# Kernel optimization log

Hardware: AMD Instinct MI355X
Metric: run time of the kernel (lower is better)

The kernel has to match this reference:

```python
import jax, jax.numpy as jnp
import numpy as np
import math

P, DD, N, E, NDRUGS = 256, 128, 1024, 250000, 200000
BASELINE = 6.0

def _prelu(x, a):
    return jnp.where(x >= 0, x, a * x)

def _lrelu(x):
    return jnp.where(x >= 0, x, 0.2 * x)

def _lin(x, W, b):
    return x @ W.T + b

def setup_inputs() -> dict:
    key = jax.random.key(0)
    ks = jax.random.split(key, 40)
    f32 = jnp.float32
    inp = {}
    inp["target_features"] = jax.random.normal(ks[0], (P,), f32)
    inp["form_features"] = jax.random.normal(ks[1], (N, P), f32)
    inp["role_features"] = jax.random.normal(ks[2], (N, P), f32)
    inp["form_neighbors"] = jnp.arange(N, dtype=jnp.int32)
    inp["form_binds_src"] = jax.random.randint(ks[3], (E,), 0, N, jnp.int32)
    inp["form_binds_dst"] = jax.random.randint(ks[4], (E,), 0, NDRUGS, jnp.int32)
    inp["form_binds_y"] = jax.random.uniform(ks[5], (E,), f32, 4.0, 9.0)
    inp["role_neighbors"] = jnp.arange(N, dtype=jnp.int32)
    inp["role_binds_src"] = jax.random.randint(ks[6], (E,), 0, N, jnp.int32)
    inp["role_binds_dst"] = jax.random.randint(ks[7], (E,), 0, NDRUGS, jnp.int32)
    inp["role_binds_y"] = jax.random.uniform(ks[8], (E,), f32, 4.0, 9.0)
    inp["drug_features"] = jax.random.normal(ks[9], (NDRUGS, DD), f32)
    s = 0.02
    # prot_refiner: Linear(P,P) -> PReLU -> Linear(P,P)
    inp["Wr1"] = jax.random.normal(ks[10], (P, P), f32) * s
    inp["br1"] = jnp.zeros((P,), f32)
    inp["ar1"] = jnp.asarray(0.25, f32)
    inp["Wr2"] = jax.random.normal(ks[11], (P, P), f32) * s
    inp["br2"] = jnp.zeros((P,), f32)
    # q/k/v projections
    inp["Wq"] = jax.random.normal(ks[12], (DD, P), f32) * s
    inp["bq"] = jnp.zeros((DD,), f32)
    inp["Wk"] = jax.random.normal(ks[13], (DD, DD), f32) * s
    inp["bk"] = jnp.zeros((DD,), f32)
    inp["Wv"] = jax.random.normal(ks[14], (DD, DD), f32) * s
    inp["bv"] = jnp.zeros((DD,), f32)
    inp["layer_emb"] = jax.random.normal(ks[15], (2, 16), f32) * s
    # attn_net: (2P+16)->128->64->1 with LeakyReLU(0.2)
    inp["Wa1"] = jax.random.normal(ks[16], (128, 2 * P + 16), f32) * s
    inp["ba1"] = jnp.zeros((128,), f32)
    inp["Wa2"] = jax.random.normal(ks[17], (64, 128), f32) * s
    inp["ba2"] = jnp.zeros((64,), f32)
    inp["Wa3"] = jax.random.normal(ks[18], (1, 64), f32) * s
    inp["ba3"] = jnp.zeros((1,), f32)
    # integration_mlp: Linear(DD,P) -> PReLU -> Linear(P,P)
    inp["Wi1"] = jax.random.normal(ks[19], (P, DD), f32) * s
    inp["bi1"] = jnp.zeros((P,), f32)
    inp["ai"] = jnp.asarray(0.25, f32)
    inp["Wi2"] = jax.random.normal(ks[20], (P, P), f32) * s
    inp["bi2"] = jnp.zeros((P,), f32)
    inp["ln_g"] = jnp.ones((P,), f32)
    inp["ln_b"] = jnp.zeros((P,), f32)
    return inp

def reference(target_features, form_features, role_features, form_neighbors,
              form_binds_src, form_binds_dst, form_binds_y,
              role_neighbors, role_binds_src, role_binds_dst, role_binds_y,
              drug_features,
              Wr1, br1, ar1, Wr2, br2, Wq, bq, Wk, bk, Wv, bv, layer_emb,
              Wa1, ba1, Wa2, ba2, Wa3, ba3, Wi1, bi1, ai, Wi2, bi2, ln_g, ln_b):
    def refine(x):
        return _lin(_prelu(_lin(x, Wr1, br1), ar1), Wr2, br2)

    zt = refine(target_features)          # [P]
    zf = refine(form_features)            # [N, P]
    zr = refine(role_features)            # [N, P]
    Qv = _lin(zt, Wq, bq)                 # [DD]

    def build_msgs(neighbors, src, dst, y):
        # segment id for each edge: position of src in (sorted) neighbor_ids;
        # edges whose src is not a neighbor go to the dummy segment n.
        n = neighbors.shape[0]
        pos = jnp.clip(jnp.searchsorted(neighbors, src), 0, n - 1)
        seg = jnp.where(neighbors[pos] == src, pos, n)
        d = drug_features[dst]                                # [E, DD] gather
        K = _lin(d, Wk, bk)                                   # [E, DD]
        V = _lin(d, Wv, bv) * (y - BASELINE)[:, None]         # [E, DD]
        s = (K @ Qv) / math.sqrt(DD)                          # [E]
        nseg = n + 1
        m = jax.ops.segment_max(s, seg, num_segments=nseg)    # per-neighbor max
        ex = jnp.exp(s - m[seg])                              # stable softmax numerator
        den = jax.ops.segment_sum(ex, seg, num_segments=nseg)[:n]          # [N]
        num = jax.ops.segment_sum(ex[:, None] * V, seg, num_segments=nseg)[:n]  # [N, DD]
        return jnp.where(den[:, None] > 0, num / jnp.maximum(den, 1e-30)[:, None], 0.0)

    form_msgs = build_msgs(form_neighbors, form_binds_src, form_binds_dst, form_binds_y)
    role_msgs = build_msgs(role_neighbors, role_binds_src, role_binds_dst, role_binds_y)

    def attn(zn, layer_id):
        n = zn.shape[0]
        le = jnp.broadcast_to(layer_emb[layer_id], (n, 16))
        zt_e = jnp.broadcast_to(zt, (n, P))
        x = jnp.concatenate([zt_e, zn, le], axis=-1)          # [N, 2P+16]
        h = _lrelu(_lin(x, Wa1, ba1))
        h = _lrelu(_lin(h, Wa2, ba2))
        return _lin(h, Wa3, ba3)                              # [N, 1]

    all_msgs = jnp.concatenate([form_msgs, role_msgs], axis=0)   # [2N, DD]
    all_attn = jnp.concatenate([attn(zf, 0), attn(zr, 1)], axis=0)  # [2N, 1]
    w = jax.nn.softmax(all_attn, axis=0)
    v_prior = jnp.sum(w * all_msgs, axis=0)                   # [DD]
    integ = _lin(_prelu(_lin(v_prior, Wi1, bi1), ai), Wi2, bi2)
    x = zt + integ
    mu = jnp.mean(x, axis=-1, keepdims=True)
    var = jnp.var(x, axis=-1, keepdims=True)
    z = (x - mu) / jnp.sqrt(var + 1e-5) * ln_g + ln_b
    return (z, form_msgs, role_msgs)
```

## Files before the change

### kernel.cpp

```cpp
#include <hip/hip_runtime.h>

#define NP 256
#define NDD 128
#define NN 1024
#define NE 250000
#define SB 62

__global__ __launch_bounds__(256) void refine_qk_kernel(
    const float* __restrict__ tgt, const float* __restrict__ formf, const float* __restrict__ rolef,
    const float* __restrict__ Wr1, const float* __restrict__ br1, const float* __restrict__ ar1,
    const float* __restrict__ Wr2, const float* __restrict__ br2,
    const float* __restrict__ Wq, const float* __restrict__ bq,
    const float* __restrict__ Wk, const float* __restrict__ bk,
    float* __restrict__ zt, float* __restrict__ zf, float* __restrict__ zr,
    float* __restrict__ qk, float* __restrict__ s0,
    int* __restrict__ count, int* __restrict__ cursor0)
{
  __shared__ float X[4][NP];
  __shared__ float H[4][NP];
  __shared__ float Zs[NP];
  __shared__ float Q[NDD];
  __shared__ float red[NDD];
  const int t = threadIdx.x;
  const int base = blockIdx.x * 4;

  if (blockIdx.x == 1){
    #pragma unroll
    for (int i = 0; i < 8; i++) count[t + i*256] = 0;
  } else if (blockIdx.x == 2){
    #pragma unroll
    for (int i = 0; i < 8; i++) cursor0[t + i*256] = 0;
  }

  #pragma unroll
  for (int r = 0; r < 4; r++){
    int row = base + r;
    if (row < 2*NN + 1){
      const float* xp;
      if (row == 0)        xp = tgt;
      else if (row <= NN)  xp = formf + (size_t)(row-1)*NP;
      else                 xp = rolef + (size_t)(row-NN-1)*NP;
      X[r][t] = xp[t];
    } else {
      X[r][t] = 0.f;
    }
  }
  __syncthreads();
  const float a1 = ar1[0];
  float acc[4];
  #pragma unroll
  for (int r = 0; r < 4; r++) acc[r] = 0.f;
  const float4* w1p = reinterpret_cast<const float4*>(Wr1) + t*(NP/4);
  for (int k4 = 0; k4 < NP/4; k4++){
    float4 w = w1p[k4];
    #pragma unroll
    for (int r = 0; r < 4; r++){
      float4 xv = *reinterpret_cast<const float4*>(&X[r][k4*4]);
      acc[r] = fmaf(w.x, xv.x, acc[r]);
      acc[r] = fmaf(w.y, xv.y, acc[r]);
      acc[r] = fmaf(w.z, xv.z, acc[r]);
      acc[r] = fmaf(w.w, xv.w, acc[r]);
    }
  }
  const float b1 = br1[t];
  #pragma unroll
  for (int r = 0; r < 4; r++){
    float h = acc[r] + b1;
    H[r][t] = h >= 0.f ? h : a1*h;
  }
  __syncthreads();
  #pragma unroll
  for (int r = 0; r < 4; r++) acc[r] = 0.f;
  const float4* w2p = reinterpret_cast<const float4*>(Wr2) + t*(NP/4);
  for (int k4 = 0; k4 < NP/4; k4++){
    float4 w = w2p[k4];
    #pragma unroll
    for (int r = 0; r < 4; r++){
      float4 hv = *reinterpret_cast<const float4*>(&H[r][k4*4]);
      acc[r] = fmaf(w.x, hv.x, acc[r]);
      acc[r] = fmaf(w.y, hv.y, acc[r]);
      acc[r] = fmaf(w.z, hv.z, acc[r]);
      acc[r] = fmaf(w.w, hv.w, acc[r]);
    }
  }
  const float b2 = br2[t];
  #pragma unroll
  for (int r = 0; r < 4; r++){
    int row = base + r;
    if (row < 2*NN + 1){
      float v = acc[r] + b2;
      float* op;
      if (row == 0){ op = zt; Zs[t] = v; }
      else if (row <= NN)  op = zf + (size_t)(row-1)*NP;
      else                 op = zr + (size_t)(row-NN-1)*NP;
      op[t] = v;
    }
  }

  if (blockIdx.x == 0){
    __syncthreads();
    if (t < NDD){
      float a = 0.f;
      const float4* wq = reinterpret_cast<const float4*>(Wq) + t*(NP/4);
      for (int k4 = 0; k4 < NP/4; k4++){
        float4 w = wq[k4];
        float4 zv = *reinterpret_cast<const float4*>(&Zs[k4*4]);
        a = fmaf(w.x, zv.x, fmaf(w.y, zv.y, fmaf(w.z, zv.z, fmaf(w.w, zv.w, a))));
      }
      float qv = a + bq[t];
      Q[t] = qv;
      red[t] = bk[t] * qv;
    }
    __syncthreads();
    const float rs = 0.08838834764831845f;
    if (t < NDD){
      float a2 = 0.f;
      for (int j = 0; j < NDD; j++) a2 = fmaf(Wk[j*NDD + t], Q[j], a2);
      qk[t] = a2 * rs;
    }
    for (int o = 64; o; o >>= 1){
      if (t < o) red[t] += red[t+o];
      __syncthreads();
    }
    if (t == 0) s0[0] = red[0] * rs;
  }
}

__device__ __forceinline__ int seg_of(const int* NB, int s){
  if ((unsigned)s < NN && NB[s] == s) return s;
  int lo = 0, hi = NN;
  while (lo < hi){ int mid = (lo+hi)>>1; if (NB[mid] < s) lo = mid+1; else hi = mid; }
  return lo < NN ? lo : NN-1;
}

__global__ __launch_bounds__(1024) void hist_kernel(
    const int* __restrict__ neighF, const int* __restrict__ srcF,
    const int* __restrict__ neighR, const int* __restrict__ srcR,
    int* __restrict__ count)
{
  __shared__ int NB[NN];
  __shared__ int lh[NN];
  int bi = blockIdx.x;
  int role = bi >= SB ? 1 : 0;
  int blk = bi - role*SB;
  const int* neigh = role ? neighR : neighF;
  const int* src   = role ? srcR   : srcF;
  int* cnt = count + role*NN;
  int t = threadIdx.x;
  NB[t] = neigh[t];
  lh[t] = 0;
  __syncthreads();
  #pragma unroll
  for (int i = 0; i < 4; i++){
    int e = blk*4096 + i*1024 + t;
    if (e < NE){
      int s = src[e];
      int pos = seg_of(NB, s);
      if (NB[pos] == s) atomicAdd(&lh[pos], 1);
    }
  }
  __syncthreads();
  int c = lh[t];
  if (c > 0) atomicAdd(&cnt[t], c);
}

__global__ __launch_bounds__(1024) void scatter_kernel(
    const int* __restrict__ neighF, const int* __restrict__ srcF,
    const int* __restrict__ dstF, const float* __restrict__ yF,
    const int* __restrict__ neighR, const int* __restrict__ srcR,
    const int* __restrict__ dstR, const float* __restrict__ yR,
    const int* __restrict__ count, int* __restrict__ cursor0,
    int* __restrict__ offsets, int2* __restrict__ edges)
{
  __shared__ int NB[NN];
  __shared__ int lcur[NN];
  __shared__ int sscan[NN];
  __shared__ int obase[NN];
  __shared__ int lbase[NN];
  int bi = blockIdx.x;
  int role = bi >= SB ? 1 : 0;
  int blk = bi - role*SB;
  const int* neigh = role ? neighR : neighF;
  const int* src   = role ? srcR   : srcF;
  const int* dst   = role ? dstR   : dstF;
  const float* yb  = role ? yR     : yF;
  int* cur0 = cursor0 + role*NN;
  int2* ed  = edges   + (size_t)role*NE;
  int t = threadIdx.x;
  NB[t] = neigh[t];
  lcur[t] = 0;
  int c0 = count[role*NN + t];
  sscan[t] = c0;
  __syncthreads();
  for (int o = 1; o < NN; o <<= 1){
    int v = (t >= o) ? sscan[t-o] : 0;
    __syncthreads();
    sscan[t] += v;
    __syncthreads();
  }
  obase[t] = sscan[t] - c0;
  if (blk == 0) offsets[role*NN + t] = sscan[t] - c0;
  __syncthreads();

  int segr[4], locr[4]; int2 edr[4];
  #pragma unroll
  for (int i = 0; i < 4; i++){
    int e = blk*4096 + i*1024 + t;
    segr[i] = -1;
    if (e < NE){
      int s = src[e];
      int pos = seg_of(NB, s);
      if (NB[pos] == s){
        segr[i] = pos;
        edr[i]  = make_int2(dst[e], __float_as_int(yb[e]));
        locr[i] = atomicAdd(&lcur[pos], 1);
      }
    }
  }
  __syncthreads();
  int c = lcur[t];
  if (c > 0) lbase[t] = obase[t] + atomicAdd(&cur0[t], c);
  __syncthreads();
  #pragma unroll
  for (int i = 0; i < 4; i++){
    if (segr[i] >= 0){
      ed[(size_t)(lbase[segr[i]] + locr[i])] = edr[i];
    }
  }
}

__global__ __launch_bounds__(256) void seg_kernel(
    const float* __restrict__ drug,
    const int2* __restrict__ edges,
    const int* __restrict__ offsets, const int* __restrict__ count,
    const float* __restrict__ qk, const float* __restrict__ s0p,
    float* __restrict__ g, float* __restrict__ den, float* __restrict__ cfac)
{
  int b = blockIdx.x;
  int tid = threadIdx.x;
  int w = tid >> 6, lane = tid & 63, l32 = lane & 31, half = lane >> 5;
  int off = offsets[b], cnt = count[b];
  int l = b >> 10;
  const int2* eb = edges + (size_t)l*NE;
  float4 q = reinterpret_cast<const float4*>(qk)[l32];
  float s0 = s0p[0];
  int chunk = (cnt + 3) >> 2;
  int start = w*chunk;
  int end = min(start + chunk, cnt);
  float dn = 0.f, cc = 0.f;
  float4 ga = make_float4(0.f,0.f,0.f,0.f);
  for (int i = start; i < end; i += 8){
    int dstp[4]; float yp[4]; bool vp[4];
    #pragma unroll
    for (int p2 = 0; p2 < 4; p2++){
      int idx = i + 2*p2 + half;
      bool v = idx < end;
      int2 e = eb[off + (v ? idx : start)];
      dstp[p2] = e.x; yp[p2] = __int_as_float(e.y); vp[p2] = v;
    }
    float4 dv[4];
    #pragma unroll
    for (int p2 = 0; p2 < 4; p2++){
      dv[p2] = reinterpret_cast<const float4*>(drug + (size_t)dstp[p2]*NDD)[l32];
    }
    #pragma unroll
    for (int p2 = 0; p2 < 4; p2++){
      float4 d = dv[p2];
      float s = fmaf(d.x, q.x, fmaf(d.y, q.y, fmaf(d.z, q.z, d.w*q.w)));
      s += __shfl_xor(s, 16, 64);
      s += __shfl_xor(s,  8, 64);
      s += __shfl_xor(s,  4, 64);
      s += __shfl_xor(s,  2, 64);
      s += __shfl_xor(s,  1, 64);
      float ex = vp[p2] ? __expf(s + s0) : 0.f;
      float wv = ex * (yp[p2] - 6.0f);
      dn += ex; cc += wv;
      ga.x = fmaf(wv, d.x, ga.x);
      ga.y = fmaf(wv, d.y, ga.y);
      ga.z = fmaf(wv, d.z, ga.z);
      ga.w = fmaf(wv, d.w, ga.w);
    }
  }
  __shared__ float4 sG[8][32];
  __shared__ float sD[8], sC[8];
  int slot = w*2 + half;
  sG[slot][l32] = ga;
  if (l32 == 0){ sD[slot] = dn; sC[slot] = cc; }
  __syncthreads();
  if (tid < NDD){
    int a = tid >> 2, c = tid & 3;
    float v = 0.f;
    #pragma unroll
    for (int k = 0; k < 8; k++)
      v += reinterpret_cast<const float*>(&sG[k][a])[c];
    g[(size_t)b*NDD + tid] = v;
    if (tid == 0){
      float ds = 0.f, cs = 0.f;
      #pragma unroll
      for (int k = 0; k < 8; k++){ ds += sD[k]; cs += sC[k]; }
      den[b] = ds; cfac[b] = cs;
    }
  }
}

__global__ __launch_bounds__(256) void attn_msgs_kernel(
    const float* __restrict__ zt, const float* __restrict__ zf, const float* __restrict__ zr,
    const float* __restrict__ lemb,
    const float* __restrict__ Wa1, const float* __restrict__ ba1,
    const float* __restrict__ Wa2, const float* __restrict__ ba2,
    const float* __restrict__ Wa3, const float* __restrict__ ba3,
    const float* __restrict__ g, const float* __restrict__ den, const float* __restrict__ cfac,
    const float* __restrict__ Wv, const float* __restrict__ bv,
    float* __restrict__ attn, float* __restrict__ msgsf, float* __restrict__ outm)
{
  int t = threadIdx.x;
  int tt = t & 127, grp = t >> 7;
  if (blockIdx.x < 256){
    __shared__ float X[8][528];
    __shared__ float H1[8][NDD];
    int base = blockIdx.x*8;
    for (int r = 0; r < 8; r++){
      int i = base + r;
      int layer = i >> 10, nn = i & (NN-1);
      const float* zn = (layer == 0) ? (zf + (size_t)nn*NP) : (zr + (size_t)nn*NP);
      for (int idx = t; idx < 528; idx += 256){
        float v;
        if (idx < NP)        v = zt[idx];
        else if (idx < 2*NP) v = zn[idx - NP];
        else                 v = lemb[layer*16 + (idx - 2*NP)];
        X[r][idx] = v;
      }
    }
    __syncthreads();
    float acc[4];
    #pragma unroll
    for (int r = 0; r < 4; r++) acc[r] = 0.f;
    const float4* w1 = reinterpret_cast<const float4*>(Wa1) + tt*(528/4);
    for (int k4 = 0; k4 < 132; k4++){
      float4 w = w1[k4];
      #pragma unroll
      for (int r = 0; r < 4; r++){
        float4 xv = *reinterpret_cast<const float4*>(&X[grp*4 + r][k4*4]);
        acc[r] = fmaf(w.x, xv.x, acc[r]);
        acc[r] = fmaf(w.y, xv.y, acc[r]);
        acc[r] = fmaf(w.z, xv.z, acc[r]);
        acc[r] = fmaf(w.w, xv.w, acc[r]);
      }
    }
    float b1 = ba1[tt];
    #pragma unroll
    for (int r = 0; r < 4; r++){
      float h = acc[r] + b1;
      H1[grp*4 + r][tt] = h >= 0.f ? h : 0.2f*h;
    }
    __syncthreads();
    if (tt < 64){
      float acc2[4];
      #pragma unroll
      for (int r = 0; r < 4; r++) acc2[r] = 0.f;
      const float4* w2 = reinterpret_cast<const float4*>(Wa2) + tt*(NDD/4);
      for (int k4 = 0; k4 < NDD/4; k4++){
        float4 w = w2[k4];
        #pragma unroll
        for (int r = 0; r < 4; r++){
          float4 hv = *reinterpret_cast<const float4*>(&H1[grp*4 + r][k4*4]);
          acc2[r] = fmaf(w.x, hv.x, acc2[r]);
          acc2[r] = fmaf(w.y, hv.y, acc2[r]);
          acc2[r] = fmaf(w.z, hv.z, acc2[r]);
          acc2[r] = fmaf(w.w, hv.w, acc2[r]);
        }
      }
      float b2 = ba2[tt];
      float w3 = Wa3[tt];
      float b3 = ba3[0];
      #pragma unroll
      for (int r = 0; r < 4; r++){
        float h = acc2[r] + b2;
        h = h >= 0.f ? h : 0.2f*h;
        float p = w3 * h;
        #pragma unroll
        for (int o = 32; o; o >>= 1) p += __shfl_xor(p, o, 64);
        if (tt == 0) attn[base + grp*4 + r] = p + b3;
      }
    }
  } else {
    __shared__ float G[8][NDD];
    int base = (blockIdx.x - 256)*8;
    #pragma unroll
    for (int r = 0; r < 4; r++) G[grp*4 + r][tt] = g[(size_t)(base + grp*4 + r)*NDD + tt];
    __syncthreads();
    float acc[4];
    #pragma unroll
    for (int r = 0; r < 4; r++) acc[r] = 0.f;
    const float4* wv4 = reinterpret_cast<const float4*>(Wv) + tt*(NDD/4);
    for (int k4 = 0; k4 < NDD/4; k4++){
      float4 w = wv4[k4];
      #pragma unroll
      for (int r = 0; r < 4; r++){
        float4 gv = *reinterpret_cast<const float4*>(&G[grp*4 + r][k4*4]);
        acc[r] = fmaf(w.x, gv.x, acc[r]);
        acc[r] = fmaf(w.y, gv.y, acc[r]);
        acc[r] = fmaf(w.z, gv.z, acc[r]);
        acc[r] = fmaf(w.w, gv.w, acc[r]);
      }
    }
    float bvj = bv[tt];
    #pragma unroll
    for (int r = 0; r < 4; r++){
      int row = base + grp*4 + r;
      float dn = den[row];
      float v = 0.f;
      if (dn > 0.f) v = (acc[r] + bvj*cfac[row]) / fmaxf(dn, 1e-30f);
      msgsf[(size_t)row*NDD + tt] = v;
      outm [(size_t)row*NDD + tt] = v;
    }
  }
}

__global__ __launch_bounds__(1024) void vprior_final_kernel(
    const float* __restrict__ attn, const float* __restrict__ msgsf,
    const float* __restrict__ zt,
    const float* __restrict__ Wi1, const float* __restrict__ bi1, const float* __restrict__ ai,
    const float* __restrict__ Wi2, const float* __restrict__ bi2,
    const float* __restrict__ ln_g, const float* __restrict__ ln_b,
    float* __restrict__ zout)
{
  __shared__ float A[2*NN];
  __shared__ float red[1024];
  __shared__ float Pp[8][NDD];
  __shared__ float V[NDD];
  __shared__ float T1[NP];
  __shared__ float red2[NP];
  int t = threadIdx.x;
  A[t] = attn[t]; A[t+1024] = attn[t+1024];
  __syncthreads();
  float mx = fmaxf(A[t], A[t+1024]);
  red[t] = mx; __syncthreads();
  for (int o = 512; o; o >>= 1){ if (t < o) red[t] = fmaxf(red[t], red[t+o]); __syncthreads(); }
  float M = red[0]; __syncthreads();
  float sm = __expf(A[t] - M) + __expf(A[t+1024] - M);
  red[t] = sm; __syncthreads();
  for (int o = 512; o; o >>= 1){ if (t < o) red[t] += red[t+o]; __syncthreads(); }
  float inv = 1.f / red[0]; __syncthreads();
  A[t]      = __expf(A[t]      - M) * inv;
  A[t+1024] = __expf(A[t+1024] - M) * inv;
  __syncthreads();
  int j = t & 127, grp = t >> 7;
  float acc = 0.f;
  int i0 = grp * 256;
  for (int i = i0; i < i0 + 256; i++) acc = fmaf(A[i], msgsf[(size_t)i*NDD + j], acc);
  Pp[grp][j] = acc;
  __syncthreads();
  if (t < NDD){
    float v = 0.f;
    #pragma unroll
    for (int gg = 0; gg < 8; gg++) v += Pp[gg][t];
    V[t] = v;
  }
  __syncthreads();
  float x = 0.f;
  if (t < NP){
    float a1 = 0.f;
    const float4* w1 = reinterpret_cast<const float4*>(Wi1) + t*(NDD/4);
    for (int k4 = 0; k4 < NDD/4; k4++){
      float4 w = w1[k4];
      float4 vv = *reinterpret_cast<const float4*>(&V[k4*4]);
      a1 = fmaf(w.x, vv.x, fmaf(w.y, vv.y, fmaf(w.z, vv.z, fmaf(w.w, vv.w, a1))));
    }
    float h = a1 + bi1[t];
    float a = ai[0];
    T1[t] = h >= 0.f ? h : a*h;
  }
  __syncthreads();
  if (t < NP){
    float a2 = 0.f;
    const float4* w2 = reinterpret_cast<const float4*>(Wi2) + t*(NP/4);
    for (int k4 = 0; k4 < NP/4; k4++){
      float4 w = w2[k4];
      float4 hv = *reinterpret_cast<const float4*>(&T1[k4*4]);
      a2 = fmaf(w.x, hv.x, fmaf(w.y, hv.y, fmaf(w.z, hv.z, fmaf(w.w, hv.w, a2))));
    }
    x = zt[t] + a2 + bi2[t];
    red2[t] = x;
  }
  __syncthreads();
  for (int o = 128; o; o >>= 1){ if (t < o) red2[t] += red2[t+o]; __syncthreads(); }
  float mu = red2[0] * (1.f/256.f); __syncthreads();
  float d = x - mu;
  if (t < NP) red2[t] = d*d;
  __syncthreads();
  for (int o = 128; o; o >>= 1){ if (t < o) red2[t] += red2[t+o]; __syncthreads(); }
  if (t < NP){
    float var = red2[0] * (1.f/256.f);
    float zz = d * rsqrtf(var + 1e-5f) * ln_g[t] + ln_b[t];
    zout[t] = zz;
  }
}

extern "C" void kernel_launch(void* const* d_in, const int* in_sizes, int n_in,
                              void* d_out, int out_size, void* d_ws, size_t ws_size,
                              hipStream_t stream)
{
  const float* tgt    = (const float*)d_in[0];
  const float* formf  = (const float*)d_in[1];
  const float* rolef  = (const float*)d_in[2];
  const int* fneigh   = (const int*)d_in[3];
  const int* fsrc     = (const int*)d_in[4];
  const int* fdst     = (const int*)d_in[5];
  const float* fy     = (const float*)d_in[6];
  const int* rneigh   = (const int*)d_in[7];
  const int* rsrc     = (const int*)d_in[8];
  const int* rdst     = (const int*)d_in[9];
  const float* ry     = (const float*)d_in[10];
  const float* drug   = (const float*)d_in[11];
  const float* Wr1 = (const float*)d_in[12];
  const float* br1 = (const float*)d_in[13];
  const float* ar1 = (const float*)d_in[14];
  const float* Wr2 = (const float*)d_in[15];
  const float* br2 = (const float*)d_in[16];
  const float* Wq  = (const float*)d_in[17];
  const float* bq  = (const float*)d_in[18];
  const float* Wk  = (const float*)d_in[19];
  const float* bk  = (const float*)d_in[20];
  const float* Wv  = (const float*)d_in[21];
  const float* bv  = (const float*)d_in[22];
  const float* lemb= (const float*)d_in[23];
  const float* Wa1 = (const float*)d_in[24];
  const float* ba1 = (const float*)d_in[25];
  const float* Wa2 = (const float*)d_in[26];
  const float* ba2 = (const float*)d_in[27];
  const float* Wa3 = (const float*)d_in[28];
  const float* ba3 = (const float*)d_in[29];
  const float* Wi1 = (const float*)d_in[30];
  const float* bi1 = (const float*)d_in[31];
  const float* ai  = (const float*)d_in[32];
  const float* Wi2 = (const float*)d_in[33];
  const float* bi2 = (const float*)d_in[34];
  const float* lng = (const float*)d_in[35];
  const float* lnb = (const float*)d_in[36];
  (void)in_sizes; (void)n_in; (void)out_size; (void)ws_size;

  float* ws = (float*)d_ws;
  float* zt_     = ws + 0;
  float* zf_     = ws + 256;
  float* zr_     = ws + 262400;
  float* qk_     = ws + 524544;
  float* s0_     = ws + 524672;
  float* attn_   = ws + 524800;
  float* den_    = ws + 527104;
  float* cfac_   = ws + 529152;
  float* g_      = ws + 531200;
  float* msgsf_  = ws + 793344;
  int*   count_  = (int*)(ws + 1055488);
  int*   offs_   = (int*)(ws + 1057536);
  int*   cursor_ = (int*)(ws + 1059584);
  int2*  edges_  = (int2*)(ws + 1061632);

  refine_qk_kernel<<<513, 256, 0, stream>>>(tgt, formf, rolef, Wr1, br1, ar1, Wr2, br2,
                                            Wq, bq, Wk, bk,
                                            zt_, zf_, zr_, qk_, s0_, count_, cursor_);

  hist_kernel<<<2*SB, 1024, 0, stream>>>(fneigh, fsrc, rneigh, rsrc, count_);
  scatter_kernel<<<2*SB, 1024, 0, stream>>>(fneigh, fsrc, fdst, fy,
                                            rneigh, rsrc, rdst, ry,
                                            count_, cursor_, offs_, edges_);

  seg_kernel<<<2*NN, 256, 0, stream>>>(drug, edges_, offs_, count_, qk_, s0_,
                                       g_, den_, cfac_);

  attn_msgs_kernel<<<512, 256, 0, stream>>>(zt_, zf_, zr_, lemb,
                                            Wa1, ba1, Wa2, ba2, Wa3, ba3,
                                            g_, den_, cfac_, Wv, bv,
                                            attn_, msgsf_, (float*)d_out + NP);
  vprior_final_kernel<<<1, 1024, 0, stream>>>(attn_, msgsf_, zt_,
                                              Wi1, bi1, ai, Wi2, bi2,
                                              lng, lnb, (float*)d_out);
}
```

Measured before the change: 392.4 us.

## Fuse histogram into refine kernel, raise rows per block, memset counters

Merges the edge histogram pass into the protein-refiner kernel as extra blocks, so the two independent stages share one launch and run concurrently. Refiner blocks now process 16 rows instead of 4, which improves reuse of each weight load at the cost of more registers and shared memory. Counter and cursor zeroing moves to a hipMemsetAsync, which also clears offsets. Histogram blocks shrink to 256 threads, each handling 16 edges.

```diff
diff --git a/kernel.cpp b/kernel.cpp
--- a/kernel.cpp
+++ b/kernel.cpp
@@ -5,35 +5,69 @@
 #define NN 1024
 #define NE 250000
 #define SB 62
-
-__global__ __launch_bounds__(256) void refine_qk_kernel(
+#define RB 129
+
+__global__ __launch_bounds__(256) void refine_qk_hist_kernel(
     const float* __restrict__ tgt, const float* __restrict__ formf, const float* __restrict__ rolef,
     const float* __restrict__ Wr1, const float* __restrict__ br1, const float* __restrict__ ar1,
     const float* __restrict__ Wr2, const float* __restrict__ br2,
     const float* __restrict__ Wq, const float* __restrict__ bq,
     const float* __restrict__ Wk, const float* __restrict__ bk,
+    const int* __restrict__ neighF, const int* __restrict__ srcF,
+    const int* __restrict__ neighR, const int* __restrict__ srcR,
     float* __restrict__ zt, float* __restrict__ zf, float* __restrict__ zr,
     float* __restrict__ qk, float* __restrict__ s0,
-    int* __restrict__ count, int* __restrict__ cursor0)
+    int* __restrict__ count)
 {
-  __shared__ float X[4][NP];
-  __shared__ float H[4][NP];
+  __shared__ float X[16][NP];
+  __shared__ float H[16][NP];
   __shared__ float Zs[NP];
   __shared__ float Q[NDD];
   __shared__ float red[NDD];
   const int t = threadIdx.x;
-  const int base = blockIdx.x * 4;
-
-  if (blockIdx.x == 1){
-    #pragma unroll
-    for (int i = 0; i < 8; i++) count[t + i*256] = 0;
-  } else if (blockIdx.x == 2){
-    #pragma unroll
-    for (int i = 0; i < 8; i++) cursor0[t + i*256] = 0;
-  }
-
-  #pragma unroll
-  for (int r = 0; r < 4; r++){
+
+  if (blockIdx.x >= RB){
+    int bi = blockIdx.x - RB;
+    int role = bi >= SB ? 1 : 0;
+    int blk = bi - role*SB;
+    const int* neigh = role ? neighR : neighF;
+    const int* src   = role ? srcR   : srcF;
+    int* cnt = count + role*NN;
+    int* NB = (int*)&X[0][0];
+    int* lh = NB + NN;
+    #pragma unroll
+    for (int i = 0; i < NN/256; i++){
+      NB[t + i*256] = neigh[t + i*256];
+      lh[t + i*256] = 0;
+    }
+    __syncthreads();
+    #pragma unroll
+    for (int i = 0; i < 16; i++){
+      int e = blk*4096 + i*256 + t;
+      if (e < NE){
+        int s = src[e];
+        int pos;
+        if ((unsigned)s < NN && NB[s] == s) pos = s;
+        else {
+          int lo = 0, hi = NN;
+          while (lo < hi){ int mid = (lo+hi)>>1; if (NB[mid] < s) lo = mid+1; else hi = mid; }
+          pos = lo < NN ? lo : NN-1;
+        }
+        if (NB[pos] == s) atomicAdd(&lh[pos], 1);
+      }
+    }
+    __syncthreads();
+    #pragma unroll
+    for (int i = 0; i < NN/256; i++){
+      int c = lh[t + i*256];
+      if (c > 0) atomicAdd(&cnt[t + i*256], c);
+    }
+    return;
+  }
+
+  const int base = blockIdx.x * 16;
+  #pragma unroll
+  for (int r = 0; r < 16; r++){
     int row = base + r;
     if (row < 2*NN + 1){
       const float* xp;
@@ -47,14 +81,14 @@
   }
   __syncthreads();
   const float a1 = ar1[0];
-  float acc[4];
-  #pragma unroll
-  for (int r = 0; r < 4; r++) acc[r] = 0.f;
+  float acc[16];
+  #pragma unroll
+  for (int r = 0; r < 16; r++) acc[r] = 0.f;
   const float4* w1p = reinterpret_cast<const float4*>(Wr1) + t*(NP/4);
   for (int k4 = 0; k4 < NP/4; k4++){
     float4 w = w1p[k4];
     #pragma unroll
-    for (int r = 0; r < 4; r++){
+    for (int r = 0; r < 16; r++){
       float4 xv = *reinterpret_cast<const float4*>(&X[r][k4*4]);
       acc[r] = fmaf(w.x, xv.x, acc[r]);
       acc[r] = fmaf(w.y, xv.y, acc[r]);
@@ -64,18 +98,18 @@
   }
   const float b1 = br1[t];
   #pragma unroll
-  for (int r = 0; r < 4; r++){
+  for (int r = 0; r < 16; r++){
     float h = acc[r] + b1;
     H[r][t] = h >= 0.f ? h : a1*h;
   }
   __syncthreads();
   #pragma unroll
-  for (int r = 0; r < 4; r++) acc[r] = 0.f;
+  for (int r = 0; r < 16; r++) acc[r] = 0.f;
   const float4* w2p = reinterpret_cast<const float4*>(Wr2) + t*(NP/4);
   for (int k4 = 0; k4 < NP/4; k4++){
     float4 w = w2p[k4];
     #pragma unroll
-    for (int r = 0; r < 4; r++){
+    for (int r = 0; r < 16; r++){
       float4 hv = *reinterpret_cast<const float4*>(&H[r][k4*4]);
       acc[r] = fmaf(w.x, hv.x, acc[r]);
       acc[r] = fmaf(w.y, hv.y, acc[r]);
@@ -85,7 +119,7 @@
   }
   const float b2 = br2[t];
   #pragma unroll
-  for (int r = 0; r < 4; r++){
+  for (int r = 0; r < 16; r++){
     int row = base + r;
     if (row < 2*NN + 1){
       float v = acc[r] + b2;
@@ -131,37 +165,6 @@
   int lo = 0, hi = NN;
   while (lo < hi){ int mid = (lo+hi)>>1; if (NB[mid] < s) lo = mid+1; else hi = mid; }
   return lo < NN ? lo : NN-1;
-}
-
-__global__ __launch_bounds__(1024) void hist_kernel(
-    const int* __restrict__ neighF, const int* __restrict__ srcF,
-    const int* __restrict__ neighR, const int* __restrict__ srcR,
-    int* __restrict__ count)
-{
-  __shared__ int NB[NN];
-  __shared__ int lh[NN];
-  int bi = blockIdx.x;
-  int role = bi >= SB ? 1 : 0;
-  int blk = bi - role*SB;
-  const int* neigh = role ? neighR : neighF;
-  const int* src   = role ? srcR   : srcF;
-  int* cnt = count + role*NN;
-  int t = threadIdx.x;
-  NB[t] = neigh[t];
-  lh[t] = 0;
-  __syncthreads();
-  #pragma unroll
-  for (int i = 0; i < 4; i++){
-    int e = blk*4096 + i*1024 + t;
-    if (e < NE){
-      int s = src[e];
-      int pos = seg_of(NB, s);
-      if (NB[pos] == s) atomicAdd(&lh[pos], 1);
-    }
-  }
-  __syncthreads();
-  int c = lh[t];
-  if (c > 0) atomicAdd(&cnt[t], c);
 }
 
 __global__ __launch_bounds__(1024) void scatter_kernel(
@@ -556,11 +559,13 @@
   int*   cursor_ = (int*)(ws + 1059584);
   int2*  edges_  = (int2*)(ws + 1061632);
 
-  refine_qk_kernel<<<513, 256, 0, stream>>>(tgt, formf, rolef, Wr1, br1, ar1, Wr2, br2,
-                                            Wq, bq, Wk, bk,
-                                            zt_, zf_, zr_, qk_, s0_, count_, cursor_);
-
-  hist_kernel<<<2*SB, 1024, 0, stream>>>(fneigh, fsrc, rneigh, rsrc, count_);
+  hipMemsetAsync(count_, 0, 3*2*NN*sizeof(int), stream);
+
+  refine_qk_hist_kernel<<<RB + 2*SB, 256, 0, stream>>>(
+      tgt, formf, rolef, Wr1, br1, ar1, Wr2, br2, Wq, bq, Wk, bk,
+      fneigh, fsrc, rneigh, rsrc,
+      zt_, zf_, zr_, qk_, s0_, count_);
+
   scatter_kernel<<<2*SB, 1024, 0, stream>>>(fneigh, fsrc, fdst, fy,
                                             rneigh, rsrc, rdst, ry,
                                             count_, cursor_, offs_, edges_);
```

Result: no change. 390.8 us (-0.4%).
